# Kernel tuning notes

Measured on AMD Instinct MI355X. Metric: run time of the kernel, lower is better.

Reference implementation:

```python
import jax, jax.numpy as jnp
import numpy as np

N_NODES = 100000
N_EDGES = 1600000
IN_DIM = 128
HID = 64
N_CLASSES = 40
NEG_SLOPE = 0.2


def setup_inputs() -> dict:
    key = jax.random.key(0)
    ks = jax.random.split(key, 12)
    s_in = 1.0 / np.sqrt(IN_DIM)
    s_h = 1.0 / np.sqrt(HID)
    return {
        "x": jax.random.normal(ks[0], (N_NODES, IN_DIM), dtype=jnp.float32),
        "edge_index": jax.random.randint(ks[1], (2, N_EDGES), 0, N_NODES, dtype=jnp.int64),
        "W0": jax.random.normal(ks[2], (IN_DIM, HID), dtype=jnp.float32) * s_in,
        "a_s0": jax.random.normal(ks[3], (HID,), dtype=jnp.float32) * s_h,
        "a_d0": jax.random.normal(ks[4], (HID,), dtype=jnp.float32) * s_h,
        "b0": jnp.zeros((HID,), dtype=jnp.float32),
        "W1": jax.random.normal(ks[5], (HID, HID), dtype=jnp.float32) * s_h,
        "a_s1": jax.random.normal(ks[6], (HID,), dtype=jnp.float32) * s_h,
        "a_d1": jax.random.normal(ks[7], (HID,), dtype=jnp.float32) * s_h,
        "b1": jnp.zeros((HID,), dtype=jnp.float32),
        "Wl": jax.random.normal(ks[8], (HID, N_CLASSES), dtype=jnp.float32) * s_h,
        "bl": jnp.zeros((N_CLASSES,), dtype=jnp.float32),
    }


def gat_conv(x, src, dst, W, a_s, a_d, b, n_nodes):
    # single-head GATConv (PyG default heads=1), self-loops already in src/dst
    h = x @ W                                  # [N, d]
    e = jax.nn.leaky_relu((h @ a_s)[src] + (h @ a_d)[dst], NEG_SLOPE)  # [E]
    # segment softmax over incoming edges of each dst node
    m = jax.ops.segment_max(e, dst, num_segments=n_nodes)
    p = jnp.exp(e - m[dst])
    denom = jax.ops.segment_sum(p, dst, num_segments=n_nodes)
    alpha = p / (denom[dst] + 1e-16)           # [E]
    out = jax.ops.segment_sum(alpha[:, None] * h[src], dst, num_segments=n_nodes)
    return out + b


def reference(x, edge_index, W0, a_s0, a_d0, b0, W1, a_s1, a_d1, b1, Wl, bl):
    n = x.shape[0]
    loop = jnp.arange(n, dtype=edge_index.dtype)
    src = jnp.concatenate([edge_index[0], loop])
    dst = jnp.concatenate([edge_index[1], loop])
    h = gat_conv(x, src, dst, W0, a_s0, a_d0, b0, n)
    h = jax.nn.elu(h)
    h = gat_conv(h, src, dst, W1, a_s1, a_d1, b1, n)
    h = jax.nn.elu(h)
    return h @ Wl + bl
```

## Files before the change

### kernel.cpp

```cpp
#include <hip/hip_runtime.h>
#include <math.h>

#define NEG_SLOPE 0.2f
#define CAP 256
#define BSH 9
#define BSZ 512
#define CHUNK 2048
#define PADS 16
#define HGRID 256

typedef __attribute__((ext_vector_type(8))) short short8;
typedef __attribute__((ext_vector_type(4))) float f32x4;

__device__ __forceinline__ float hred_sum(float v) {
#pragma unroll
    for (int o = 16; o >= 1; o >>= 1) v += __shfl_xor(v, o, 64);
    return v;
}
__device__ __forceinline__ unsigned int f2bf(float f) {
    unsigned int u = __float_as_uint(f);
    return (u + 0x7fffu + ((u >> 16) & 1u)) >> 16;
}
__device__ __forceinline__ float bflo(unsigned int u) { return __uint_as_float(u << 16); }
__device__ __forceinline__ float bfhi(unsigned int u) { return __uint_as_float(u & 0xffff0000u); }


__global__ __launch_bounds__(256) void k_hist(const int* __restrict__ dst, int* __restrict__ bpart, int E) {
    __shared__ int lh[256];
    lh[threadIdx.x] = 0;
    __syncthreads();
    int gid = blockIdx.x * 256 + threadIdx.x;
    int nth = gridDim.x * 256;
    int E4 = E >> 2;
    for (int i = gid; i < E4; i += nth) {
        int4 d = ((const int4*)dst)[i];
        atomicAdd(&lh[d.x >> BSH], 1);
        atomicAdd(&lh[d.y >> BSH], 1);
        atomicAdd(&lh[d.z >> BSH], 1);
        atomicAdd(&lh[d.w >> BSH], 1);
    }
    for (int i = (E4 << 2) + gid; i < E; i += nth)
        atomicAdd(&lh[dst[i] >> BSH], 1);
    __syncthreads();
    bpart[blockIdx.x * 256 + threadIdx.x] = lh[threadIdx.x];
}

__global__ __launch_bounds__(256) void k_bscan(const int* __restrict__ bpart,
                                               int* __restrict__ eoff, int* __restrict__ boff,
                                               int* __restrict__ bcursor, int* __restrict__ ecnt,
                                               int* __restrict__ rowptr,
                                               int nbuck, int N, int E) {
    __shared__ int s1[256], s2[256];
    int t = threadIdx.x;
    int bc = 0;
    for (int b = 0; b < HGRID; b += 4) {
        bc += bpart[(b + 0) * 256 + t];
        bc += bpart[(b + 1) * 256 + t];
        bc += bpart[(b + 2) * 256 + t];
        bc += bpart[(b + 3) * 256 + t];
    }
    if (t >= nbuck) bc = 0;
    int cn = 0;
    if (t < nbuck) { cn = N - (t << BSH); if (cn > BSZ) cn = BSZ; if (cn < 0) cn = 0; }
    int tot = bc + cn;
    s1[t] = bc; s2[t] = tot;
    __syncthreads();
#pragma unroll
    for (int off = 1; off < 256; off <<= 1) {
        int u1 = (t >= off) ? s1[t - off] : 0;
        int u2 = (t >= off) ? s2[t - off] : 0;
        __syncthreads();
        s1[t] += u1; s2[t] += u2;
        __syncthreads();
    }
    if (t < nbuck) {
        int e = s1[t] - bc, b = s2[t] - tot;
        eoff[t] = e; boff[t] = b; ecnt[t] = bc; bcursor[t * PADS] = e;
    }
    if (t == 0) rowptr[N] = E + N;
}

__global__ __launch_bounds__(256) void k_scatter(const int* __restrict__ src, const int* __restrict__ dst,
                                                 int* __restrict__ bcursor, int* __restrict__ ebuf, int E) {
    __shared__ int lh[256], lb[256];
    const int tid = threadIdx.x;
    int base = blockIdx.x * CHUNK;
    int sv[8], dv[8];
    bool ok[8];
#pragma unroll
    for (int u = 0; u < 8; ++u) {
        int i = base + u * 256 + tid;
        ok[u] = i < E;
        int ii = ok[u] ? i : E - 1;
        dv[u] = dst[ii];
        sv[u] = src[ii];
    }
    lh[tid] = 0;
    __syncthreads();
#pragma unroll
    for (int u = 0; u < 8; ++u)
        if (ok[u]) atomicAdd(&lh[dv[u] >> BSH], 1);
    __syncthreads();
    int c = lh[tid];
    lb[tid] = c ? atomicAdd(&bcursor[tid * PADS], c) : 0;
    lh[tid] = 0;
    __syncthreads();
#pragma unroll
    for (int u = 0; u < 8; ++u) {
        if (ok[u]) {
            int d = dv[u], b = d >> BSH;
            int p = atomicAdd(&lh[b], 1);
            ebuf[lb[b] + p] = (sv[u] << BSH) | (d & (BSZ - 1));
        }
    }
}

__global__ __launch_bounds__(512) void k_build(const int* __restrict__ eoff, const int* __restrict__ boff,
                                               const int* __restrict__ ecnt, const int* __restrict__ ebuf,
                                               int* __restrict__ rowptr, int* __restrict__ csr, int N) {
    __shared__ int sdeg[BSZ], sscan[BSZ];
    int b = blockIdx.x, t = threadIdx.x;
    int nlo = b << BSH;
    int cn = N - nlo; if (cn > BSZ) cn = BSZ;
    int e0 = eoff[b], ec = ecnt[b], cb = boff[b];
    sdeg[t] = (t < cn) ? 1 : 0;
    __syncthreads();
    {
        int i = t;
        for (; i + 1536 < ec; i += 2048) {
            int r0 = ebuf[e0 + i], r1 = ebuf[e0 + i + 512];
            int r2 = ebuf[e0 + i + 1024], r3 = ebuf[e0 + i + 1536];
            atomicAdd(&sdeg[r0 & (BSZ - 1)], 1);
            atomicAdd(&sdeg[r1 & (BSZ - 1)], 1);
            atomicAdd(&sdeg[r2 & (BSZ - 1)], 1);
            atomicAdd(&sdeg[r3 & (BSZ - 1)], 1);
        }
        for (; i < ec; i += 512)
            atomicAdd(&sdeg[ebuf[e0 + i] & (BSZ - 1)], 1);
    }
    __syncthreads();
    int v = sdeg[t];
    sscan[t] = v;
    __syncthreads();
#pragma unroll
    for (int off = 1; off < BSZ; off <<= 1) {
        int u = (t >= off) ? sscan[t - off] : 0;
        __syncthreads();
        sscan[t] += u;
        __syncthreads();
    }
    int excl = sscan[t] - v;
    if (t < cn) {
        rowptr[nlo + t] = cb + excl;
        csr[cb + excl] = nlo + t;
        sdeg[t] = excl + 1;
    }
    __syncthreads();
    {
        int i = t;
        for (; i + 1536 < ec; i += 2048) {
            int r0 = ebuf[e0 + i], r1 = ebuf[e0 + i + 512];
            int r2 = ebuf[e0 + i + 1024], r3 = ebuf[e0 + i + 1536];
            int p0 = atomicAdd(&sdeg[r0 & (BSZ - 1)], 1);
            int p1 = atomicAdd(&sdeg[r1 & (BSZ - 1)], 1);
            int p2 = atomicAdd(&sdeg[r2 & (BSZ - 1)], 1);
            int p3 = atomicAdd(&sdeg[r3 & (BSZ - 1)], 1);
            csr[cb + p0] = r0 >> BSH;
            csr[cb + p1] = r1 >> BSH;
            csr[cb + p2] = r2 >> BSH;
            csr[cb + p3] = r3 >> BSH;
        }
        for (; i < ec; i += 512) {
            int rec = ebuf[e0 + i];
            int p = atomicAdd(&sdeg[rec & (BSZ - 1)], 1);
            csr[cb + p] = rec >> BSH;
        }
    }
}


template <int K, int OUTW, bool SS, bool HB, bool XB>
__global__ __launch_bounds__(256) void k_gemm(const void* __restrict__ X,
                                              const float* __restrict__ W,
                                              const float* __restrict__ a_s,
                                              const float* __restrict__ a_d,
                                              const float* __restrict__ bias,
                                              void* __restrict__ Hout,
                                              float* __restrict__ ss,
                                              float* __restrict__ sd, int N) {
    constexpr int NKC = K / 32;
    constexpr int NC  = (OUTW + 15) / 16;
    __shared__ __align__(16) short wfrag[NKC * NC * 64 * 8];
    __shared__ __align__(16) unsigned int hs[HB ? 4 : 1][16 * 32];

    const int tid  = threadIdx.x;
    const int lane = tid & 63;
    const int w    = tid >> 6;
    const int m    = lane & 15;
    const int q8   = lane >> 4;
    const int rowbase = blockIdx.x * 64 + w * 16;

    for (int f = tid; f < NKC * NC * 64; f += 256) {
        int flane = f & 63;
        int fc    = (f >> 6) % NC;
        int fkc   = (f >> 6) / NC;
        int col   = fc * 16 + (flane & 15);
        int k0    = fkc * 32 + (flane >> 4) * 8;
        short8 b;
#pragma unroll
        for (int j = 0; j < 8; ++j) {
            float v = (col < OUTW) ? W[(k0 + j) * OUTW + col] : 0.f;
            b[j] = (short)f2bf(v);
        }
        *(short8*)&wfrag[f * 8] = b;
    }
    __syncthreads();

    int grow = rowbase + m; if (grow >= N) grow = N - 1;

    f32x4 acc[NC];
#pragma unroll
    for (int c = 0; c < NC; ++c) acc[c] = (f32x4)0.f;

    if (XB) {
        const unsigned short* xrow = (const unsigned short*)X + (size_t)grow * 64 + q8 * 8;
#pragma unroll
        for (int kc = 0; kc < NKC; ++kc) {
            short8 ah = *(const short8*)(xrow + kc * 32);
#pragma unroll
            for (int c = 0; c < NC; ++c) {
                short8 b = *(short8*)&wfrag[((kc * NC + c) * 64 + lane) * 8];
                acc[c] = __builtin_amdgcn_mfma_f32_16x16x32_bf16(ah, b, acc[c], 0, 0, 0);
            }
        }
    } else {
        const float* xrow = (const float*)X + (size_t)grow * K + q8 * 8;
#pragma unroll
        for (int kc = 0; kc < NKC; ++kc) {
            float4 v0 = *(const float4*)(xrow + kc * 32);
            float4 v1 = *(const float4*)(xrow + kc * 32 + 4);
            float vv[8] = {v0.x, v0.y, v0.z, v0.w, v1.x, v1.y, v1.z, v1.w};
            short8 ah, al;
#pragma unroll
            for (int j = 0; j < 8; ++j) {
                unsigned int hb16 = f2bf(vv[j]);
                ah[j] = (short)hb16;
                al[j] = (short)f2bf(vv[j] - __uint_as_float(hb16 << 16));
            }
#pragma unroll
            for (int c = 0; c < NC; ++c) {
                short8 b = *(short8*)&wfrag[((kc * NC + c) * 64 + lane) * 8];
                acc[c] = __builtin_amdgcn_mfma_f32_16x16x32_bf16(ah, b, acc[c], 0, 0, 0);
                acc[c] = __builtin_amdgcn_mfma_f32_16x16x32_bf16(al, b, acc[c], 0, 0, 0);
            }
        }
    }

    if (SS) {
        float asv[NC], adv[NC];
#pragma unroll
        for (int c = 0; c < NC; ++c) { asv[c] = a_s[c * 16 + m]; adv[c] = a_d[c * 16 + m]; }
#pragma unroll
        for (int i = 0; i < 4; ++i) {
            float s = 0.f, d = 0.f;
#pragma unroll
            for (int c = 0; c < NC; ++c) {
                s = fmaf(acc[c][i], asv[c], s);
                d = fmaf(acc[c][i], adv[c], d);
            }
#pragma unroll
            for (int o = 1; o <= 8; o <<= 1) {
                s += __shfl_xor(s, o, 64);
                d += __shfl_xor(d, o, 64);
            }
            int r = rowbase + q8 * 4 + i;
            if (m == 0 && r < N) { ss[r] = s; sd[r] = d; }
        }
    }

    if (HB) {
        unsigned short* hsw = (unsigned short*)&hs[w][0];
#pragma unroll
        for (int c = 0; c < NC; ++c)
#pragma unroll
            for (int i = 0; i < 4; ++i)
                hsw[(q8 * 4 + i) * 64 + c * 16 + m] = (unsigned short)f2bf(acc[c][i]);
        unsigned int* hu = &hs[w][0];
        int row = lane >> 2, u0 = (lane & 3) * 8;
        uint4 va = *(uint4*)&hu[row * 32 + u0];
        uint4 vb = *(uint4*)&hu[row * 32 + u0 + 4];
        int r = rowbase + row;
        if (r < N) {
            unsigned int* hbp = (unsigned int*)Hout;
            *(uint4*)&hbp[(size_t)r * 32 + u0]     = va;
            *(uint4*)&hbp[(size_t)r * 32 + u0 + 4] = vb;
        }
    } else {
        float bv[NC];
#pragma unroll
        for (int c = 0; c < NC; ++c) {
            int col = c * 16 + m;
            bv[c] = (col < OUTW) ? bias[col] : 0.f;
        }
        float* O = (float*)Hout;
#pragma unroll
        for (int i = 0; i < 4; ++i) {
            int r = rowbase + q8 * 4 + i;
            if (r < N) {
#pragma unroll
                for (int c = 0; c < NC; ++c) {
                    int col = c * 16 + m;
                    if (col < OUTW) O[(size_t)r * OUTW + col] = acc[c][i] + bv[c];
                }
            }
        }
    }
}


__global__ __launch_bounds__(256) void k_agg(const int* __restrict__ rowptr, const int* __restrict__ csr,
                                             const float* __restrict__ ss, const float* __restrict__ sd,
                                             const unsigned int* __restrict__ hb, const float* __restrict__ bias,
                                             unsigned int* __restrict__ z, int N) {
    __shared__ __align__(16) float sal[8][CAP];
    __shared__ __align__(16) int   sof[8][CAP];
    const int tid = threadIdx.x;
    const int hw  = tid >> 5;
    const int p   = tid & 31;
    const int n   = blockIdx.x * 8 + hw;
    const bool valid = n < N;
    const char* hbb = (const char*)hb;
    const int p4 = p * 4;

    int ro = 0, deg = 0;
    float sdn = 0.f;
    if (valid) {
        ro  = rowptr[n];
        deg = rowptr[n + 1] - ro;
        sdn = sd[n];
    }

    if (deg <= CAP) {
        float sum = 0.f;
        for (int j = p; j < deg; j += 32) {
            int s = csr[ro + j];
            float e = ss[s] + sdn;
            e = fmaxf(e, NEG_SLOPE * e);
            float pe = __expf(e);
            sal[hw][j] = pe;
            sof[hw][j] = s << 7;
            sum += pe;
        }
        sum = hred_sum(sum);
        float inv = 1.f / (sum + 1e-16f);

        float ax = 0.f, ay = 0.f, bx = 0.f, by = 0.f, cx = 0.f, cy = 0.f, dx = 0.f, dy = 0.f;
        int j = 0;
        for (; j + 7 < deg; j += 8) {
            float4 al0 = *(const float4*)&sal[hw][j];
            float4 al1 = *(const float4*)&sal[hw][j + 4];
            int4   of0 = *(const int4*)&sof[hw][j];
            int4   of1 = *(const int4*)&sof[hw][j + 4];
            unsigned int u0 = *(const unsigned int*)(hbb + (of0.x + p4));
            unsigned int u1 = *(const unsigned int*)(hbb + (of0.y + p4));
            unsigned int u2 = *(const unsigned int*)(hbb + (of0.z + p4));
            unsigned int u3 = *(const unsigned int*)(hbb + (of0.w + p4));
            unsigned int u4 = *(const unsigned int*)(hbb + (of1.x + p4));
            unsigned int u5 = *(const unsigned int*)(hbb + (of1.y + p4));
            unsigned int u6 = *(const unsigned int*)(hbb + (of1.z + p4));
            unsigned int u7 = *(const unsigned int*)(hbb + (of1.w + p4));
            ax = fmaf(bflo(u0), al0.x, ax); ay = fmaf(bfhi(u0), al0.x, ay);
            bx = fmaf(bflo(u1), al0.y, bx); by = fmaf(bfhi(u1), al0.y, by);
            cx = fmaf(bflo(u2), al0.z, cx); cy = fmaf(bfhi(u2), al0.z, cy);
            dx = fmaf(bflo(u3), al0.w, dx); dy = fmaf(bfhi(u3), al0.w, dy);
            ax = fmaf(bflo(u4), al1.x, ax); ay = fmaf(bfhi(u4), al1.x, ay);
            bx = fmaf(bflo(u5), al1.y, bx); by = fmaf(bfhi(u5), al1.y, by);
            cx = fmaf(bflo(u6), al1.z, cx); cy = fmaf(bfhi(u6), al1.z, cy);
            dx = fmaf(bflo(u7), al1.w, dx); dy = fmaf(bfhi(u7), al1.w, dy);
        }
        for (; j + 3 < deg; j += 4) {
            float4 al0 = *(const float4*)&sal[hw][j];
            int4   of0 = *(const int4*)&sof[hw][j];
            unsigned int u0 = *(const unsigned int*)(hbb + (of0.x + p4));
            unsigned int u1 = *(const unsigned int*)(hbb + (of0.y + p4));
            unsigned int u2 = *(const unsigned int*)(hbb + (of0.z + p4));
            unsigned int u3 = *(const unsigned int*)(hbb + (of0.w + p4));
            ax = fmaf(bflo(u0), al0.x, ax); ay = fmaf(bfhi(u0), al0.x, ay);
            bx = fmaf(bflo(u1), al0.y, bx); by = fmaf(bfhi(u1), al0.y, by);
            cx = fmaf(bflo(u2), al0.z, cx); cy = fmaf(bfhi(u2), al0.z, cy);
            dx = fmaf(bflo(u3), al0.w, dx); dy = fmaf(bfhi(u3), al0.w, dy);
        }
        for (; j < deg; ++j) {
            float a = sal[hw][j];
            unsigned int u0 = *(const unsigned int*)(hbb + (sof[hw][j] + p4));
            ax = fmaf(bflo(u0), a, ax); ay = fmaf(bfhi(u0), a, ay);
        }
        float fx = (ax + bx) + (cx + dx);
        float fy = (ay + by) + (cy + dy);
        if (valid) {
            float2 ob = *(const float2*)&bias[p * 2];
            float ox = fmaf(fx, inv, ob.x);
            float oy = fmaf(fy, inv, ob.y);
            ox = (ox > 0.f) ? ox : __expf(ox) - 1.f;
            oy = (oy > 0.f) ? oy : __expf(oy) - 1.f;
            z[(size_t)n * 32 + p] = (f2bf(oy) << 16) | f2bf(ox);
        }
    } else {
        float sum = 0.f;
        for (int j = p; j < deg; j += 32) {
            int s = csr[ro + j];
            float e = ss[s] + sdn;
            e = fmaxf(e, NEG_SLOPE * e);
            sum += __expf(e);
        }
        sum = hred_sum(sum);
        float inv = 1.f / (sum + 1e-16f);
        float fx = 0.f, fy = 0.f;
        for (int j = 0; j < deg; ++j) {
            int s = csr[ro + j];
            float e = ss[s] + sdn;
            e = fmaxf(e, NEG_SLOPE * e);
            float pe = __expf(e);
            unsigned int u = *(const unsigned int*)(hbb + ((s << 7) + p4));
            fx = fmaf(bflo(u), pe, fx); fy = fmaf(bfhi(u), pe, fy);
        }
        float2 ob = *(const float2*)&bias[p * 2];
        float ox = fmaf(fx, inv, ob.x);
        float oy = fmaf(fy, inv, ob.y);
        ox = (ox > 0.f) ? ox : __expf(ox) - 1.f;
        oy = (oy > 0.f) ? oy : __expf(oy) - 1.f;
        z[(size_t)n * 32 + p] = (f2bf(oy) << 16) | f2bf(ox);
    }
}


extern "C" void kernel_launch(void* const* d_in, const int* in_sizes, int n_in,
                              void* d_out, int out_size, void* d_ws, size_t ws_size,
                              hipStream_t stream) {
    const float* x   = (const float*)d_in[0];
    const int*   ei  = (const int*)d_in[1];
    const float* W0  = (const float*)d_in[2];
    const float* as0 = (const float*)d_in[3];
    const float* ad0 = (const float*)d_in[4];
    const float* b0  = (const float*)d_in[5];
    const float* W1  = (const float*)d_in[6];
    const float* as1 = (const float*)d_in[7];
    const float* ad1 = (const float*)d_in[8];
    const float* b1  = (const float*)d_in[9];
    const float* Wl  = (const float*)d_in[10];
    const float* bl  = (const float*)d_in[11];
    float* out = (float*)d_out;

    int N = in_sizes[0] / 128;
    int E = in_sizes[1] / 2;
    const int* srcp = ei;
    const int* dstp = ei + E;
    int nbuck = (N + BSZ - 1) >> BSH;

    char* wp = (char*)d_ws;
    auto alloc = [&](size_t bytes) { void* p = (void*)wp; wp += (bytes + 255) & ~(size_t)255; return p; };
    unsigned int* hb = (unsigned int*)alloc((size_t)N * 32 * 4);
    unsigned int* z  = (unsigned int*)alloc((size_t)N * 32 * 4);
    float* ssb     = (float*)alloc((size_t)N * 4);
    float* sdb     = (float*)alloc((size_t)N * 4);
    int*   rowptr  = (int*)alloc((size_t)(N + 1) * 4);
    int*   csr     = (int*)alloc((size_t)(E + N) * 4);
    int*   ebuf    = (int*)alloc((size_t)E * 4);
    int*   bpart   = (int*)alloc((size_t)HGRID * 256 * 4);
    int*   eoff    = (int*)alloc(256 * 4);
    int*   boff    = (int*)alloc(256 * 4);
    int*   ecnt    = (int*)alloc(256 * 4);
    int*   bcursor = (int*)alloc(256 * PADS * 4);

    k_hist<<<HGRID, 256, 0, stream>>>(dstp, bpart, E);
    k_bscan<<<1, 256, 0, stream>>>(bpart, eoff, boff, bcursor, ecnt, rowptr, nbuck, N, E);
    k_scatter<<<(E + CHUNK - 1) / CHUNK, 256, 0, stream>>>(srcp, dstp, bcursor, ebuf, E);
    k_build<<<nbuck, 512, 0, stream>>>(eoff, boff, ecnt, ebuf, rowptr, csr, N);

    int gb = (N + 63) / 64;
    k_gemm<128, 64, true, true, false><<<gb, 256, 0, stream>>>(x, W0, as0, ad0, nullptr, hb, ssb, sdb, N);
    k_agg<<<(N + 7) / 8, 256, 0, stream>>>(rowptr, csr, ssb, sdb, hb, b0, z, N);
    k_gemm<64, 64, true, true, true><<<gb, 256, 0, stream>>>(z, W1, as1, ad1, nullptr, hb, ssb, sdb, N);
    k_agg<<<(N + 7) / 8, 256, 0, stream>>>(rowptr, csr, ssb, sdb, hb, b1, z, N);
    k_gemm<64, 40, false, false, true><<<gb, 256, 0, stream>>>(z, Wl, nullptr, nullptr, bl, out, nullptr, nullptr, N);
}
```

Measured before the change: 266.6 us.

## Fuse scatter with first GEMM and fold next-layer GEMV into aggregation

The edge scatter and the first-layer GEMM are merged into one launch with block-index dispatch, so they run concurrently. The aggregation kernel now also does the following dense layer (W1 or Wl) as a per-node GEMV through warp shuffles against bf16 weights held in shared memory. It also computes the next layer's attention scores, which removes two GEMM launches and the round trip of the intermediate z array. CAP is halved to cut shared memory and raise occupancy, at the cost of more time spent in the slow path for high-degree nodes, plus lower weight precision and extra per-node ALU work.

```diff
diff --git a/kernel.cpp b/kernel.cpp
--- a/kernel.cpp
+++ b/kernel.cpp
@@ -2,7 +2,7 @@
 #include <math.h>
 
 #define NEG_SLOPE 0.2f
-#define CAP 256
+#define CAP 128
 #define BSH 9
 #define BSZ 512
 #define CHUNK 2048
@@ -80,11 +80,14 @@
     if (t == 0) rowptr[N] = E + N;
 }
 
-__global__ __launch_bounds__(256) void k_scatter(const int* __restrict__ src, const int* __restrict__ dst,
-                                                 int* __restrict__ bcursor, int* __restrict__ ebuf, int E) {
-    __shared__ int lh[256], lb[256];
+
+__device__ __forceinline__ void scatter_body(char* smem, int bid,
+        const int* __restrict__ src, const int* __restrict__ dst,
+        int* __restrict__ bcursor, int* __restrict__ ebuf, int E) {
+    int* lh = (int*)smem;
+    int* lb = lh + 256;
     const int tid = threadIdx.x;
-    int base = blockIdx.x * CHUNK;
+    int base = bid * CHUNK;
     int sv[8], dv[8];
     bool ok[8];
 #pragma unroll
@@ -109,10 +112,115 @@
     for (int u = 0; u < 8; ++u) {
         if (ok[u]) {
             int d = dv[u], b = d >> BSH;
-            int p = atomicAdd(&lh[b], 1);
-            ebuf[lb[b] + p] = (sv[u] << BSH) | (d & (BSZ - 1));
-        }
-    }
+            int pp = atomicAdd(&lh[b], 1);
+            ebuf[lb[b] + pp] = (sv[u] << BSH) | (d & (BSZ - 1));
+        }
+    }
+}
+
+__device__ __forceinline__ void gemm0_body(char* smem, int bid,
+        const float* __restrict__ X, const float* __restrict__ W,
+        const float* __restrict__ a_s, const float* __restrict__ a_d,
+        unsigned int* __restrict__ hb, float* __restrict__ ss, float* __restrict__ sd, int N) {
+    constexpr int K = 128, OUTW = 64, NKC = K / 32, NC = OUTW / 16;
+    short* wfrag = (short*)smem;
+    unsigned int* hs = (unsigned int*)(smem + NKC * NC * 64 * 8 * 2);
+
+    const int tid  = threadIdx.x;
+    const int lane = tid & 63;
+    const int w    = tid >> 6;
+    const int m    = lane & 15;
+    const int q8   = lane >> 4;
+    const int rowbase = bid * 64 + w * 16;
+
+    for (int f = tid; f < NKC * NC * 64; f += 256) {
+        int flane = f & 63;
+        int fc    = (f >> 6) % NC;
+        int fkc   = (f >> 6) / NC;
+        int col   = fc * 16 + (flane & 15);
+        int k0    = fkc * 32 + (flane >> 4) * 8;
+        short8 b;
+#pragma unroll
+        for (int j = 0; j < 8; ++j) b[j] = (short)f2bf(W[(k0 + j) * OUTW + col]);
+        *(short8*)&wfrag[f * 8] = b;
+    }
+    __syncthreads();
+
+    int grow = rowbase + m; if (grow >= N) grow = N - 1;
+
+    f32x4 acc[NC];
+#pragma unroll
+    for (int c = 0; c < NC; ++c) acc[c] = (f32x4)0.f;
+
+    const float* xrow = X + (size_t)grow * K + q8 * 8;
+#pragma unroll
+    for (int kc = 0; kc < NKC; ++kc) {
+        float4 v0 = *(const float4*)(xrow + kc * 32);
+        float4 v1 = *(const float4*)(xrow + kc * 32 + 4);
+        float vv[8] = {v0.x, v0.y, v0.z, v0.w, v1.x, v1.y, v1.z, v1.w};
+        short8 ah, al;
+#pragma unroll
+        for (int j = 0; j < 8; ++j) {
+            unsigned int hb16 = f2bf(vv[j]);
+            ah[j] = (short)hb16;
+            al[j] = (short)f2bf(vv[j] - __uint_as_float(hb16 << 16));
+        }
+#pragma unroll
+        for (int c = 0; c < NC; ++c) {
+            short8 b = *(short8*)&wfrag[((kc * NC + c) * 64 + lane) * 8];
+            acc[c] = __builtin_amdgcn_mfma_f32_16x16x32_bf16(ah, b, acc[c], 0, 0, 0);
+            acc[c] = __builtin_amdgcn_mfma_f32_16x16x32_bf16(al, b, acc[c], 0, 0, 0);
+        }
+    }
+
+    float asv[NC], adv[NC];
+#pragma unroll
+    for (int c = 0; c < NC; ++c) { asv[c] = a_s[c * 16 + m]; adv[c] = a_d[c * 16 + m]; }
+#pragma unroll
+    for (int i = 0; i < 4; ++i) {
+        float s = 0.f, d = 0.f;
+#pragma unroll
+        for (int c = 0; c < NC; ++c) {
+            s = fmaf(acc[c][i], asv[c], s);
+            d = fmaf(acc[c][i], adv[c], d);
+        }
+#pragma unroll
+        for (int o = 1; o <= 8; o <<= 1) {
+            s += __shfl_xor(s, o, 64);
+            d += __shfl_xor(d, o, 64);
+        }
+        int r = rowbase + q8 * 4 + i;
+        if (m == 0 && r < N) { ss[r] = s; sd[r] = d; }
+    }
+
+    unsigned short* hsw = (unsigned short*)&hs[w * 512];
+#pragma unroll
+    for (int c = 0; c < NC; ++c)
+#pragma unroll
+        for (int i = 0; i < 4; ++i)
+            hsw[(q8 * 4 + i) * 64 + c * 16 + m] = (unsigned short)f2bf(acc[c][i]);
+    unsigned int* hu = &hs[w * 512];
+    int row = lane >> 2, u0 = (lane & 3) * 8;
+    uint4 va = *(uint4*)&hu[row * 32 + u0];
+    uint4 vb = *(uint4*)&hu[row * 32 + u0 + 4];
+    int r = rowbase + row;
+    if (r < N) {
+        *(uint4*)&hb[(size_t)r * 32 + u0]     = va;
+        *(uint4*)&hb[(size_t)r * 32 + u0 + 4] = vb;
+    }
+}
+
+__global__ __launch_bounds__(256) void k_scatter_gemm0(
+        const int* __restrict__ src, const int* __restrict__ dst,
+        int* __restrict__ bcursor, int* __restrict__ ebuf, int E, int nscat,
+        const float* __restrict__ X, const float* __restrict__ W,
+        const float* __restrict__ a_s, const float* __restrict__ a_d,
+        unsigned int* __restrict__ hb, float* __restrict__ ss, float* __restrict__ sd, int N) {
+    __shared__ __align__(16) char smem[24576];
+    if ((int)blockIdx.x < nscat)
+        scatter_body(smem, blockIdx.x, src, dst, bcursor, ebuf, E);
+    else
+        gemm0_body(smem, blockIdx.x - nscat, X, W, a_s, a_d, hb, ss, sd, N);
 }
 
 __global__ __launch_bounds__(512) void k_build(const int* __restrict__ eoff, const int* __restrict__ boff,
@@ -179,152 +287,39 @@
 }
 
 
-template <int K, int OUTW, bool SS, bool HB, bool XB>
-__global__ __launch_bounds__(256) void k_gemm(const void* __restrict__ X,
-                                              const float* __restrict__ W,
-                                              const float* __restrict__ a_s,
-                                              const float* __restrict__ a_d,
-                                              const float* __restrict__ bias,
-                                              void* __restrict__ Hout,
-                                              float* __restrict__ ss,
-                                              float* __restrict__ sd, int N) {
-    constexpr int NKC = K / 32;
-    constexpr int NC  = (OUTW + 15) / 16;
-    __shared__ __align__(16) short wfrag[NKC * NC * 64 * 8];
-    __shared__ __align__(16) unsigned int hs[HB ? 4 : 1][16 * 32];
-
-    const int tid  = threadIdx.x;
-    const int lane = tid & 63;
-    const int w    = tid >> 6;
-    const int m    = lane & 15;
-    const int q8   = lane >> 4;
-    const int rowbase = blockIdx.x * 64 + w * 16;
-
-    for (int f = tid; f < NKC * NC * 64; f += 256) {
-        int flane = f & 63;
-        int fc    = (f >> 6) % NC;
-        int fkc   = (f >> 6) / NC;
-        int col   = fc * 16 + (flane & 15);
-        int k0    = fkc * 32 + (flane >> 4) * 8;
-        short8 b;
-#pragma unroll
-        for (int j = 0; j < 8; ++j) {
-            float v = (col < OUTW) ? W[(k0 + j) * OUTW + col] : 0.f;
-            b[j] = (short)f2bf(v);
-        }
-        *(short8*)&wfrag[f * 8] = b;
-    }
-    __syncthreads();
-
-    int grow = rowbase + m; if (grow >= N) grow = N - 1;
-
-    f32x4 acc[NC];
-#pragma unroll
-    for (int c = 0; c < NC; ++c) acc[c] = (f32x4)0.f;
-
-    if (XB) {
-        const unsigned short* xrow = (const unsigned short*)X + (size_t)grow * 64 + q8 * 8;
-#pragma unroll
-        for (int kc = 0; kc < NKC; ++kc) {
-            short8 ah = *(const short8*)(xrow + kc * 32);
-#pragma unroll
-            for (int c = 0; c < NC; ++c) {
-                short8 b = *(short8*)&wfrag[((kc * NC + c) * 64 + lane) * 8];
-                acc[c] = __builtin_amdgcn_mfma_f32_16x16x32_bf16(ah, b, acc[c], 0, 0, 0);
-            }
-        }
-    } else {
-        const float* xrow = (const float*)X + (size_t)grow * K + q8 * 8;
-#pragma unroll
-        for (int kc = 0; kc < NKC; ++kc) {
-            float4 v0 = *(const float4*)(xrow + kc * 32);
-            float4 v1 = *(const float4*)(xrow + kc * 32 + 4);
-            float vv[8] = {v0.x, v0.y, v0.z, v0.w, v1.x, v1.y, v1.z, v1.w};
-            short8 ah, al;
-#pragma unroll
-            for (int j = 0; j < 8; ++j) {
-                unsigned int hb16 = f2bf(vv[j]);
-                ah[j] = (short)hb16;
-                al[j] = (short)f2bf(vv[j] - __uint_as_float(hb16 << 16));
-            }
-#pragma unroll
-            for (int c = 0; c < NC; ++c) {
-                short8 b = *(short8*)&wfrag[((kc * NC + c) * 64 + lane) * 8];
-                acc[c] = __builtin_amdgcn_mfma_f32_16x16x32_bf16(ah, b, acc[c], 0, 0, 0);
-                acc[c] = __builtin_amdgcn_mfma_f32_16x16x32_bf16(al, b, acc[c], 0, 0, 0);
-            }
-        }
-    }
-
-    if (SS) {
-        float asv[NC], adv[NC];
-#pragma unroll
-        for (int c = 0; c < NC; ++c) { asv[c] = a_s[c * 16 + m]; adv[c] = a_d[c * 16 + m]; }
-#pragma unroll
-        for (int i = 0; i < 4; ++i) {
-            float s = 0.f, d = 0.f;
-#pragma unroll
-            for (int c = 0; c < NC; ++c) {
-                s = fmaf(acc[c][i], asv[c], s);
-                d = fmaf(acc[c][i], adv[c], d);
-            }
-#pragma unroll
-            for (int o = 1; o <= 8; o <<= 1) {
-                s += __shfl_xor(s, o, 64);
-                d += __shfl_xor(d, o, 64);
-            }
-            int r = rowbase + q8 * 4 + i;
-            if (m == 0 && r < N) { ss[r] = s; sd[r] = d; }
-        }
-    }
-
-    if (HB) {
-        unsigned short* hsw = (unsigned short*)&hs[w][0];
-#pragma unroll
-        for (int c = 0; c < NC; ++c)
-#pragma unroll
-            for (int i = 0; i < 4; ++i)
-                hsw[(q8 * 4 + i) * 64 + c * 16 + m] = (unsigned short)f2bf(acc[c][i]);
-        unsigned int* hu = &hs[w][0];
-        int row = lane >> 2, u0 = (lane & 3) * 8;
-        uint4 va = *(uint4*)&hu[row * 32 + u0];
-        uint4 vb = *(uint4*)&hu[row * 32 + u0 + 4];
-        int r = rowbase + row;
-        if (r < N) {
-            unsigned int* hbp = (unsigned int*)Hout;
-            *(uint4*)&hbp[(size_t)r * 32 + u0]     = va;
-            *(uint4*)&hbp[(size_t)r * 32 + u0 + 4] = vb;
-        }
-    } else {
-        float bv[NC];
-#pragma unroll
-        for (int c = 0; c < NC; ++c) {
-            int col = c * 16 + m;
-            bv[c] = (col < OUTW) ? bias[col] : 0.f;
-        }
-        float* O = (float*)Hout;
-#pragma unroll
-        for (int i = 0; i < 4; ++i) {
-            int r = rowbase + q8 * 4 + i;
-            if (r < N) {
-#pragma unroll
-                for (int c = 0; c < NC; ++c) {
-                    int col = c * 16 + m;
-                    if (col < OUTW) O[(size_t)r * OUTW + col] = acc[c][i] + bv[c];
-                }
-            }
-        }
-    }
-}
-
-
-__global__ __launch_bounds__(256) void k_agg(const int* __restrict__ rowptr, const int* __restrict__ csr,
-                                             const float* __restrict__ ss, const float* __restrict__ sd,
-                                             const unsigned int* __restrict__ hb, const float* __restrict__ bias,
-                                             unsigned int* __restrict__ z, int N) {
+template <int OUTW, bool LAST>
+__global__ __launch_bounds__(256) void k_agg_gemv(
+        const int* __restrict__ rowptr, const int* __restrict__ csr,
+        const float* __restrict__ ss, const float* __restrict__ sd,
+        const unsigned int* __restrict__ hb, const float* __restrict__ bias,
+        const float* __restrict__ W, const float* __restrict__ as2,
+        const float* __restrict__ ad2, const float* __restrict__ bias2,
+        unsigned int* __restrict__ hbout, float* __restrict__ ssout,
+        float* __restrict__ sdout, float* __restrict__ fout, int N) {
     __shared__ __align__(16) float sal[8][CAP];
     __shared__ __align__(16) int   sof[8][CAP];
+    __shared__ __align__(16) uint2 sWq[32][32];
+
     const int tid = threadIdx.x;
+
+    for (int i = tid; i < 32 * 32; i += 256) {
+        int k = i >> 5, pp = i & 31;
+        float w00 = 0.f, w01 = 0.f, w10 = 0.f, w11 = 0.f;
+        if (2 * pp < OUTW) {
+            w00 = W[(2 * k) * OUTW + 2 * pp];
+            w10 = W[(2 * k + 1) * OUTW + 2 * pp];
+            if (2 * pp + 1 < OUTW) {
+                w01 = W[(2 * k) * OUTW + 2 * pp + 1];
+                w11 = W[(2 * k + 1) * OUTW + 2 * pp + 1];
+            }
+        }
+        uint2 wv;
+        wv.x = (f2bf(w01) << 16) | f2bf(w00);
+        wv.y = (f2bf(w11) << 16) | f2bf(w10);
+        sWq[k][pp] = wv;
+    }
+    __syncthreads();
+
     const int hw  = tid >> 5;
     const int p   = tid & 31;
     const int n   = blockIdx.x * 8 + hw;
@@ -339,6 +334,9 @@
         deg = rowptr[n + 1] - ro;
         sdn = sd[n];
     }
+
+    float2 ob = *(const float2*)&bias[p * 2];
+    float ox, oy;
 
     if (deg <= CAP) {
         float sum = 0.f;
@@ -397,14 +395,8 @@
         }
         float fx = (ax + bx) + (cx + dx);
         float fy = (ay + by) + (cy + dy);
-        if (valid) {
-            float2 ob = *(const float2*)&bias[p * 2];
-            float ox = fmaf(fx, inv, ob.x);
-            float oy = fmaf(fy, inv, ob.y);
-            ox = (ox > 0.f) ? ox : __expf(ox) - 1.f;
-            oy = (oy > 0.f) ? oy : __expf(oy) - 1.f;
-            z[(size_t)n * 32 + p] = (f2bf(oy) << 16) | f2bf(ox);
-        }
+        ox = fmaf(fx, inv, ob.x);
+        oy = fmaf(fy, inv, ob.y);
     } else {
         float sum = 0.f;
         for (int j = p; j < deg; j += 32) {
@@ -424,12 +416,42 @@
             unsigned int u = *(const unsigned int*)(hbb + ((s << 7) + p4));
             fx = fmaf(bflo(u), pe, fx); fy = fmaf(bfhi(u), pe, fy);
         }
-        float2 ob = *(const float2*)&bias[p * 2];
-        float ox = fmaf(fx, inv, ob.x);
-        float oy = fmaf(fy, inv, ob.y);
-        ox = (ox > 0.f) ? ox : __expf(ox) - 1.f;
-        oy = (oy > 0.f) ? oy : __expf(oy) - 1.f;
-        z[(size_t)n * 32 + p] = (f2bf(oy) << 16) | f2bf(ox);
+        ox = fmaf(fx, inv, ob.x);
+        oy = fmaf(fy, inv, ob.y);
+    }
+    ox = (ox > 0.f) ? ox : __expf(ox) - 1.f;
+    oy = (oy > 0.f) ? oy : __expf(oy) - 1.f;
+
+    float o0 = 0.f, o1 = 0.f;
+#pragma unroll
+    for (int k = 0; k < 32; ++k) {
+        float zx = __shfl(ox, k, 32);
+        float zy = __shfl(oy, k, 32);
+        uint2 wq = sWq[k][p];
+        o0 = fmaf(zx, bflo(wq.x), o0);
+        o1 = fmaf(zx, bfhi(wq.x), o1);
+        o0 = fmaf(zy, bflo(wq.y), o0);
+        o1 = fmaf(zy, bfhi(wq.y), o1);
+    }
+
+    if constexpr (LAST) {
+        if (valid && p < OUTW / 2) {
+            float2 ov;
+            ov.x = o0 + bias2[2 * p];
+            ov.y = o1 + bias2[2 * p + 1];
+            *(float2*)&fout[(size_t)n * OUTW + 2 * p] = ov;
+        }
+    } else {
+        float2 a2 = *(const float2*)&as2[2 * p];
+        float2 d2 = *(const float2*)&ad2[2 * p];
+        float s = fmaf(o1, a2.y, o0 * a2.x);
+        float d = fmaf(o1, d2.y, o0 * d2.x);
+        s = hred_sum(s);
+        d = hred_sum(d);
+        if (valid) {
+            if (p == 0) { ssout[n] = s; sdout[n] = d; }
+            hbout[(size_t)n * 32 + p] = (f2bf(o1) << 16) | f2bf(o0);
+        }
     }
 }
 
@@ -459,10 +481,12 @@
 
     char* wp = (char*)d_ws;
     auto alloc = [&](size_t bytes) { void* p = (void*)wp; wp += (bytes + 255) & ~(size_t)255; return p; };
-    unsigned int* hb = (unsigned int*)alloc((size_t)N * 32 * 4);
-    unsigned int* z  = (unsigned int*)alloc((size_t)N * 32 * 4);
-    float* ssb     = (float*)alloc((size_t)N * 4);
-    float* sdb     = (float*)alloc((size_t)N * 4);
+    unsigned int* hb0 = (unsigned int*)alloc((size_t)N * 32 * 4);
+    unsigned int* hb1 = (unsigned int*)alloc((size_t)N * 32 * 4);
+    float* ss0     = (float*)alloc((size_t)N * 4);
+    float* sd0     = (float*)alloc((size_t)N * 4);
+    float* ss1     = (float*)alloc((size_t)N * 4);
+    float* sd1     = (float*)alloc((size_t)N * 4);
     int*   rowptr  = (int*)alloc((size_t)(N + 1) * 4);
     int*   csr     = (int*)alloc((size_t)(E + N) * 4);
     int*   ebuf    = (int*)alloc((size_t)E * 4);
@@ -472,15 +496,19 @@
     int*   ecnt    = (int*)alloc(256 * 4);
     int*   bcursor = (int*)alloc(256 * PADS * 4);
 
+    int nscat = (E + CHUNK - 1) / CHUNK;
+    int gb = (N + 63) / 64;
+
     k_hist<<<HGRID, 256, 0, stream>>>(dstp, bpart, E);
     k_bscan<<<1, 256, 0, stream>>>(bpart, eoff, boff, bcursor, ecnt, rowptr, nbuck, N, E);
-    k_scatter<<<(E + CHUNK - 1) / CHUNK, 256, 0, stream>>>(srcp, dstp, bcursor, ebuf, E);
+    k_scatter_gemm0<<<nscat + gb, 256, 0, stream>>>(srcp, dstp, bcursor, ebuf, E, nscat,
+                                                    x, W0, as0, ad0, hb0, ss0, sd0, N);
     k_build<<<nbuck, 512, 0, stream>>>(eoff, boff, ecnt, ebuf, rowptr, csr, N);
 
-    int gb = (N + 63) / 64;
-    k_gemm<128, 64, true, true, false><<<gb, 256, 0, stream>>>(x, W0, as0, ad0, nullptr, hb, ssb, sdb, N);
-    k_agg<<<(N + 7) / 8, 256, 0, stream>>>(rowptr, csr, ssb, sdb, hb, b0, z, N);
-    k_gemm<64, 64, true, true, true><<<gb, 256, 0, stream>>>(z, W1, as1, ad1, nullptr, hb, ssb, sdb, N);
-    k_agg<<<(N + 7) / 8, 256, 0, stream>>>(rowptr, csr, ssb, sdb, hb, b1, z, N);
-    k_gemm<64, 40, false, false, true><<<gb, 256, 0, stream>>>(z, Wl, nullptr, nullptr, bl, out, nullptr, nullptr, N);
-}
+    k_agg_gemv<64, false><<<(N + 7) / 8, 256, 0, stream>>>(rowptr, csr, ss0, sd0, hb0, b0,
+                                                           W1, as1, ad1, nullptr,
+                                                           hb1, ss1, sd1, nullptr, N);
+    k_agg_gemv<40, true><<<(N + 7) / 8, 256, 0, stream>>>(rowptr, csr, ss1, sd1, hb1, b1,
+                                                          Wl, nullptr, nullptr, bl,
+                                                          nullptr, nullptr, nullptr, out, N);
+}
```

Result: slower. 487.7 us (+82.9%).

## Fuse edge scatter and first-layer GEMM into one heterogeneous launch

Applied to the files above, without the earlier changes.

Merges the edge-bucketing scatter kernel and the layer-0 feature GEMM into a single launch whose blocks branch on block index, so the two independent stages can run concurrently on the GPU. This removes one kernel launch and fills idle CUs during the atomic-heavy scatter. The GEMM body is a specialized inline copy of the existing templated GEMM. Shared memory is sized for the larger role, which may reduce occupancy for the scatter blocks.

```diff
diff --git a/kernel.cpp b/kernel.cpp
--- a/kernel.cpp
+++ b/kernel.cpp
@@ -80,11 +80,14 @@
     if (t == 0) rowptr[N] = E + N;
 }
 
-__global__ __launch_bounds__(256) void k_scatter(const int* __restrict__ src, const int* __restrict__ dst,
-                                                 int* __restrict__ bcursor, int* __restrict__ ebuf, int E) {
-    __shared__ int lh[256], lb[256];
+
+__device__ __forceinline__ void scatter_body(char* smem, int bid,
+        const int* __restrict__ src, const int* __restrict__ dst,
+        int* __restrict__ bcursor, int* __restrict__ ebuf, int E) {
+    int* lh = (int*)smem;
+    int* lb = lh + 256;
     const int tid = threadIdx.x;
-    int base = blockIdx.x * CHUNK;
+    int base = bid * CHUNK;
     int sv[8], dv[8];
     bool ok[8];
 #pragma unroll
@@ -109,10 +112,115 @@
     for (int u = 0; u < 8; ++u) {
         if (ok[u]) {
             int d = dv[u], b = d >> BSH;
-            int p = atomicAdd(&lh[b], 1);
-            ebuf[lb[b] + p] = (sv[u] << BSH) | (d & (BSZ - 1));
-        }
-    }
+            int pp = atomicAdd(&lh[b], 1);
+            ebuf[lb[b] + pp] = (sv[u] << BSH) | (d & (BSZ - 1));
+        }
+    }
+}
+
+__device__ __forceinline__ void gemm0_body(char* smem, int bid,
+        const float* __restrict__ X, const float* __restrict__ W,
+        const float* __restrict__ a_s, const float* __restrict__ a_d,
+        unsigned int* __restrict__ hb, float* __restrict__ ss, float* __restrict__ sd, int N) {
+    constexpr int K = 128, OUTW = 64, NKC = K / 32, NC = OUTW / 16;
+    short* wfrag = (short*)smem;
+    unsigned int* hs = (unsigned int*)(smem + NKC * NC * 64 * 8 * 2);
+
+    const int tid  = threadIdx.x;
+    const int lane = tid & 63;
+    const int w    = tid >> 6;
+    const int m    = lane & 15;
+    const int q8   = lane >> 4;
+    const int rowbase = bid * 64 + w * 16;
+
+    for (int f = tid; f < NKC * NC * 64; f += 256) {
+        int flane = f & 63;
+        int fc    = (f >> 6) % NC;
+        int fkc   = (f >> 6) / NC;
+        int col   = fc * 16 + (flane & 15);
+        int k0    = fkc * 32 + (flane >> 4) * 8;
+        short8 b;
+#pragma unroll
+        for (int j = 0; j < 8; ++j) b[j] = (short)f2bf(W[(k0 + j) * OUTW + col]);
+        *(short8*)&wfrag[f * 8] = b;
+    }
+    __syncthreads();
+
+    int grow = rowbase + m; if (grow >= N) grow = N - 1;
+
+    f32x4 acc[NC];
+#pragma unroll
+    for (int c = 0; c < NC; ++c) acc[c] = (f32x4)0.f;
+
+    const float* xrow = X + (size_t)grow * K + q8 * 8;
+#pragma unroll
+    for (int kc = 0; kc < NKC; ++kc) {
+        float4 v0 = *(const float4*)(xrow + kc * 32);
+        float4 v1 = *(const float4*)(xrow + kc * 32 + 4);
+        float vv[8] = {v0.x, v0.y, v0.z, v0.w, v1.x, v1.y, v1.z, v1.w};
+        short8 ah, al;
+#pragma unroll
+        for (int j = 0; j < 8; ++j) {
+            unsigned int hb16 = f2bf(vv[j]);
+            ah[j] = (short)hb16;
+            al[j] = (short)f2bf(vv[j] - __uint_as_float(hb16 << 16));
+        }
+#pragma unroll
+        for (int c = 0; c < NC; ++c) {
+            short8 b = *(short8*)&wfrag[((kc * NC + c) * 64 + lane) * 8];
+            acc[c] = __builtin_amdgcn_mfma_f32_16x16x32_bf16(ah, b, acc[c], 0, 0, 0);
+            acc[c] = __builtin_amdgcn_mfma_f32_16x16x32_bf16(al, b, acc[c], 0, 0, 0);
+        }
+    }
+
+    float asv[NC], adv[NC];
+#pragma unroll
+    for (int c = 0; c < NC; ++c) { asv[c] = a_s[c * 16 + m]; adv[c] = a_d[c * 16 + m]; }
+#pragma unroll
+    for (int i = 0; i < 4; ++i) {
+        float s = 0.f, d = 0.f;
+#pragma unroll
+        for (int c = 0; c < NC; ++c) {
+            s = fmaf(acc[c][i], asv[c], s);
+            d = fmaf(acc[c][i], adv[c], d);
+        }
+#pragma unroll
+        for (int o = 1; o <= 8; o <<= 1) {
+            s += __shfl_xor(s, o, 64);
+            d += __shfl_xor(d, o, 64);
+        }
+        int r = rowbase + q8 * 4 + i;
+        if (m == 0 && r < N) { ss[r] = s; sd[r] = d; }
+    }
+
+    unsigned short* hsw = (unsigned short*)&hs[w * 512];
+#pragma unroll
+    for (int c = 0; c < NC; ++c)
+#pragma unroll
+        for (int i = 0; i < 4; ++i)
+            hsw[(q8 * 4 + i) * 64 + c * 16 + m] = (unsigned short)f2bf(acc[c][i]);
+    unsigned int* hu = &hs[w * 512];
+    int row = lane >> 2, u0 = (lane & 3) * 8;
+    uint4 va = *(uint4*)&hu[row * 32 + u0];
+    uint4 vb = *(uint4*)&hu[row * 32 + u0 + 4];
+    int r = rowbase + row;
+    if (r < N) {
+        *(uint4*)&hb[(size_t)r * 32 + u0]     = va;
+        *(uint4*)&hb[(size_t)r * 32 + u0 + 4] = vb;
+    }
+}
+
+__global__ __launch_bounds__(256) void k_scatter_gemm0(
+        const int* __restrict__ src, const int* __restrict__ dst,
+        int* __restrict__ bcursor, int* __restrict__ ebuf, int E, int nscat,
+        const float* __restrict__ X, const float* __restrict__ W,
+        const float* __restrict__ a_s, const float* __restrict__ a_d,
+        unsigned int* __restrict__ hb, float* __restrict__ ss, float* __restrict__ sd, int N) {
+    __shared__ __align__(16) char smem[24576];
+    if ((int)blockIdx.x < nscat)
+        scatter_body(smem, blockIdx.x, src, dst, bcursor, ebuf, E);
+    else
+        gemm0_body(smem, blockIdx.x - nscat, X, W, a_s, a_d, hb, ss, sd, N);
 }
 
 __global__ __launch_bounds__(512) void k_build(const int* __restrict__ eoff, const int* __restrict__ boff,
@@ -472,13 +580,15 @@
     int*   ecnt    = (int*)alloc(256 * 4);
     int*   bcursor = (int*)alloc(256 * PADS * 4);
 
+    int nscat = (E + CHUNK - 1) / CHUNK;
+    int gb = (N + 63) / 64;
+
     k_hist<<<HGRID, 256, 0, stream>>>(dstp, bpart, E);
     k_bscan<<<1, 256, 0, stream>>>(bpart, eoff, boff, bcursor, ecnt, rowptr, nbuck, N, E);
-    k_scatter<<<(E + CHUNK - 1) / CHUNK, 256, 0, stream>>>(srcp, dstp, bcursor, ebuf, E);
+    k_scatter_gemm0<<<nscat + gb, 256, 0, stream>>>(srcp, dstp, bcursor, ebuf, E, nscat,
+                                                    x, W0, as0, ad0, hb, ssb, sdb, N);
     k_build<<<nbuck, 512, 0, stream>>>(eoff, boff, ecnt, ebuf, rowptr, csr, N);
 
-    int gb = (N + 63) / 64;
-    k_gemm<128, 64, true, true, false><<<gb, 256, 0, stream>>>(x, W0, as0, ad0, nullptr, hb, ssb, sdb, N);
     k_agg<<<(N + 7) / 8, 256, 0, stream>>>(rowptr, csr, ssb, sdb, hb, b0, z, N);
     k_gemm<64, 64, true, true, true><<<gb, 256, 0, stream>>>(z, W1, as1, ad1, nullptr, hb, ssb, sdb, N);
     k_agg<<<(N + 7) / 8, 256, 0, stream>>>(rowptr, csr, ssb, sdb, hb, b1, z, N);
```

New measurement: 264.0 us. About the same (-1.0%).
